# Kernel tuning notes

Measured on AMD Instinct MI355X. Metric: run time of the kernel, lower is better.

The kernel has to match this reference:

```python
import jax, jax.numpy as jnp
import numpy as np

EPSILON = 0.05
MAX_ITER = 50


def setup_inputs() -> dict:
    key = jax.random.key(0)
    k1, k2, k3 = jax.random.split(key, 3)
    B, N, M = 16, 2048, 2048
    cost = jax.random.uniform(k1, (B, N, M), dtype=jnp.float32)  # non-negative cost
    source_marginal = jax.random.uniform(k2, (B, N), dtype=jnp.float32)
    target_marginal = jax.random.uniform(k3, (B, M), dtype=jnp.float32)
    return {"cost": cost, "source_marginal": source_marginal, "target_marginal": target_marginal}


def reference(cost, source_marginal, target_marginal):
    # Log-domain Sinkhorn: fixed MAX_ITER iterations of dual updates.
    log_r = jnp.log(source_marginal + 1e-12)  # [B, N]
    log_c = jnp.log(target_marginal + 1e-12)  # [B, M]
    log_K = -cost / EPSILON                    # [B, N, M]

    log_u0 = jnp.zeros_like(log_r)
    log_v0 = jnp.zeros_like(log_c)

    def body(carry, _):
        log_u, log_v = carry
        log_u = log_r - jax.nn.logsumexp(log_K + log_v[:, None, :], axis=-1)
        log_v = log_c - jax.nn.logsumexp(log_K + log_u[:, :, None], axis=-2)
        return (log_u, log_v), None

    (log_u, log_v), _ = jax.lax.scan(body, (log_u0, log_v0), None, length=MAX_ITER)
    # Transport plan T = exp(log_u + log_K + log_v)
    return jnp.exp(log_u[:, :, None] + log_K + log_v[:, None, :])
```

## Files before the change

### kernel.cpp

```cpp
#include <hip/hip_runtime.h>
#include <cstdint>
#include <cstddef>

constexpr int B = 16, N = 2048, M = 2048;
constexpr int MAX_ITER = 50;
#define C2 (-28.853900817779268f)

constexpr int CHUNKS = 64;
constexpr int ROWS_PER_CHUNK = N / CHUNKS;

__device__ __forceinline__ unsigned short f2bf(float f) {
  union { float f; unsigned u; } x; x.f = f;
  unsigned r = x.u + 0x7fffu + ((x.u >> 16) & 1u);
  return (unsigned short)(r >> 16);
}
__device__ __forceinline__ float bflo(unsigned w) { union { unsigned u; float f; } x; x.u = w << 16; return x.f; }
__device__ __forceinline__ float bfhi(unsigned w) { union { unsigned u; float f; } x; x.u = w & 0xffff0000u; return x.f; }

__global__ __launch_bounds__(256) void init_K(const float* __restrict__ cost,
                                              uint4* __restrict__ K) {
  unsigned gid = blockIdx.x * 256u + threadIdx.x;
  const float4* c4 = (const float4*)cost;
  uint4 w0, w1;
  {
    float4 a = c4[(size_t)gid * 4 + 0];
    float4 b = c4[(size_t)gid * 4 + 1];
    w0.x = (unsigned)f2bf(exp2f(a.x * C2)) | ((unsigned)f2bf(exp2f(a.y * C2)) << 16);
    w0.y = (unsigned)f2bf(exp2f(a.z * C2)) | ((unsigned)f2bf(exp2f(a.w * C2)) << 16);
    w0.z = (unsigned)f2bf(exp2f(b.x * C2)) | ((unsigned)f2bf(exp2f(b.y * C2)) << 16);
    w0.w = (unsigned)f2bf(exp2f(b.z * C2)) | ((unsigned)f2bf(exp2f(b.w * C2)) << 16);
  }
  {
    float4 a = c4[(size_t)gid * 4 + 2];
    float4 b = c4[(size_t)gid * 4 + 3];
    w1.x = (unsigned)f2bf(exp2f(a.x * C2)) | ((unsigned)f2bf(exp2f(a.y * C2)) << 16);
    w1.y = (unsigned)f2bf(exp2f(a.z * C2)) | ((unsigned)f2bf(exp2f(a.w * C2)) << 16);
    w1.z = (unsigned)f2bf(exp2f(b.x * C2)) | ((unsigned)f2bf(exp2f(b.y * C2)) << 16);
    w1.w = (unsigned)f2bf(exp2f(b.z * C2)) | ((unsigned)f2bf(exp2f(b.w * C2)) << 16);
  }
  K[(size_t)gid * 2]     = w0;
  K[(size_t)gid * 2 + 1] = w1;
}

template <bool FIRST>
__global__ __launch_bounds__(256) void iter_fused(const uint4* __restrict__ K,
                                                  const float* __restrict__ r,
                                                  const float* __restrict__ v,
                                                  float* __restrict__ u_out,
                                                  float* __restrict__ part) {
  const int b = blockIdx.y, chunk = blockIdx.x;
  const int n0 = chunk * ROWS_PER_CHUNK;
  const int t = threadIdx.x;
  __shared__ float vs[M];
  __shared__ float us[ROWS_PER_CHUNK];

  if (FIRST) {
    float4 one; one.x = one.y = one.z = one.w = 1.0f;
    ((float4*)vs)[t] = one;
    ((float4*)vs)[t + 256] = one;
  } else {
    const float4* vv = (const float4*)(v + (size_t)b * M);
    ((float4*)vs)[t]       = vv[t];
    ((float4*)vs)[t + 256] = vv[t + 256];
  }
  __syncthreads();

  const int wave = t >> 6, lane = t & 63;
  float vreg[32];
#pragma unroll
  for (int it = 0; it < 4; ++it) {
    float4 a = ((const float4*)vs)[it * 128 + lane * 2];
    float4 c = ((const float4*)vs)[it * 128 + lane * 2 + 1];
    vreg[it * 8 + 0] = a.x; vreg[it * 8 + 1] = a.y; vreg[it * 8 + 2] = a.z; vreg[it * 8 + 3] = a.w;
    vreg[it * 8 + 4] = c.x; vreg[it * 8 + 5] = c.y; vreg[it * 8 + 6] = c.z; vreg[it * 8 + 7] = c.w;
  }

#pragma unroll
  for (int rr = 0; rr < ROWS_PER_CHUNK / 4; ++rr) {
    const int lrow = wave * (ROWS_PER_CHUNK / 4) + rr;
    const int row = n0 + lrow;
    const uint4* Kr = K + (size_t)(b * N + row) * (M / 8);
    float acc = 0.f;
#pragma unroll
    for (int it = 0; it < 4; ++it) {
      uint4 w = Kr[it * 64 + lane];
      acc += bflo(w.x) * vreg[it * 8 + 0] + bfhi(w.x) * vreg[it * 8 + 1]
           + bflo(w.y) * vreg[it * 8 + 2] + bfhi(w.y) * vreg[it * 8 + 3]
           + bflo(w.z) * vreg[it * 8 + 4] + bfhi(w.z) * vreg[it * 8 + 5]
           + bflo(w.w) * vreg[it * 8 + 6] + bfhi(w.w) * vreg[it * 8 + 7];
    }
#pragma unroll
    for (int off = 32; off; off >>= 1) acc += __shfl_xor(acc, off, 64);
    if (lane == 0) {
      float uval = (r[b * N + row] + 1e-12f) / acc;
      us[lrow] = uval;
      u_out[b * N + row] = uval;
    }
  }
  __syncthreads();

  float acc8[8] = {0, 0, 0, 0, 0, 0, 0, 0};
  const uint4* Kb = K + (size_t)(b * N + n0) * (M / 8) + t;
#pragma unroll 8
  for (int n = 0; n < ROWS_PER_CHUNK; ++n) {
    uint4 w = Kb[(size_t)n * (M / 8)];
    float uval = us[n];
    acc8[0] += bflo(w.x) * uval; acc8[1] += bfhi(w.x) * uval;
    acc8[2] += bflo(w.y) * uval; acc8[3] += bfhi(w.y) * uval;
    acc8[4] += bflo(w.z) * uval; acc8[5] += bfhi(w.z) * uval;
    acc8[6] += bflo(w.w) * uval; acc8[7] += bfhi(w.w) * uval;
  }
  float4* P = (float4*)(part + (size_t)(b * CHUNKS + chunk) * M) + t * 2;
  float4 o0; o0.x = acc8[0]; o0.y = acc8[1]; o0.z = acc8[2]; o0.w = acc8[3];
  float4 o1; o1.x = acc8[4]; o1.y = acc8[5]; o1.z = acc8[6]; o1.w = acc8[7];
  P[0] = o0; P[1] = o1;
}

__global__ __launch_bounds__(256) void v_fin(const float* __restrict__ part,
                                             const float* __restrict__ c,
                                             float* __restrict__ v) {
  const int g = blockIdx.x * 256 + threadIdx.x;
  const int b = g >> 11, m = g & (M - 1);
  float s = 0.f;
#pragma unroll 8
  for (int ch = 0; ch < CHUNKS; ++ch) s += part[(size_t)(b * CHUNKS + ch) * M + m];
  v[g] = (c[g] + 1e-12f) / s;
}

__global__ __launch_bounds__(256) void final_T(const float* __restrict__ cost,
                                               const float* __restrict__ u,
                                               const float* __restrict__ v,
                                               float* __restrict__ out) {
  const int b = blockIdx.z, n = blockIdx.y;
  const int m4 = blockIdx.x * 256 + threadIdx.x;
  const float un = u[b * N + n];
  float4 vv = ((const float4*)(v + (size_t)b * M))[m4];
  const size_t off = ((size_t)(b * N + n) * M) / 4 + m4;
  float4 cc = ((const float4*)cost)[off];
  float4 o;
  o.x = un * vv.x * exp2f(cc.x * C2);
  o.y = un * vv.y * exp2f(cc.y * C2);
  o.z = un * vv.z * exp2f(cc.z * C2);
  o.w = un * vv.w * exp2f(cc.w * C2);
  ((float4*)out)[off] = o;
}

__global__ __launch_bounds__(256) void init_v_only(float* __restrict__ v) {
  unsigned g = blockIdx.x * 256u + threadIdx.x;
  if (g < (unsigned)(B * M)) v[g] = 1.0f;
}

template <bool FIRST>
__global__ __launch_bounds__(256) void iter_fused_cost(const float* __restrict__ cost,
                                                       const float* __restrict__ r,
                                                       const float* __restrict__ v,
                                                       float* __restrict__ u_out,
                                                       float* __restrict__ part) {
  const int b = blockIdx.y, chunk = blockIdx.x;
  const int n0 = chunk * ROWS_PER_CHUNK;
  const int t = threadIdx.x;
  __shared__ float vs[M];
  __shared__ float us[ROWS_PER_CHUNK];
  if (FIRST) {
    float4 one; one.x = one.y = one.z = one.w = 1.0f;
    ((float4*)vs)[t] = one; ((float4*)vs)[t + 256] = one;
  } else {
    const float4* vv = (const float4*)(v + (size_t)b * M);
    ((float4*)vs)[t] = vv[t]; ((float4*)vs)[t + 256] = vv[t + 256];
  }
  __syncthreads();
  const int wave = t >> 6, lane = t & 63;
  float vreg[32];
#pragma unroll
  for (int it = 0; it < 4; ++it) {
    float4 a = ((const float4*)vs)[it * 128 + lane * 2];
    float4 c = ((const float4*)vs)[it * 128 + lane * 2 + 1];
    vreg[it * 8 + 0] = a.x; vreg[it * 8 + 1] = a.y; vreg[it * 8 + 2] = a.z; vreg[it * 8 + 3] = a.w;
    vreg[it * 8 + 4] = c.x; vreg[it * 8 + 5] = c.y; vreg[it * 8 + 6] = c.z; vreg[it * 8 + 7] = c.w;
  }
#pragma unroll
  for (int rr = 0; rr < ROWS_PER_CHUNK / 4; ++rr) {
    const int lrow = wave * (ROWS_PER_CHUNK / 4) + rr;
    const int row = n0 + lrow;
    const float4* Cr = (const float4*)(cost + (size_t)(b * N + row) * M);
    float acc = 0.f;
#pragma unroll
    for (int it = 0; it < 4; ++it) {
      float4 a = Cr[it * 128 + lane * 2];
      float4 c = Cr[it * 128 + lane * 2 + 1];
      acc += exp2f(a.x * C2) * vreg[it * 8 + 0] + exp2f(a.y * C2) * vreg[it * 8 + 1]
           + exp2f(a.z * C2) * vreg[it * 8 + 2] + exp2f(a.w * C2) * vreg[it * 8 + 3]
           + exp2f(c.x * C2) * vreg[it * 8 + 4] + exp2f(c.y * C2) * vreg[it * 8 + 5]
           + exp2f(c.z * C2) * vreg[it * 8 + 6] + exp2f(c.w * C2) * vreg[it * 8 + 7];
    }
#pragma unroll
    for (int off = 32; off; off >>= 1) acc += __shfl_xor(acc, off, 64);
    if (lane == 0) {
      float uval = (r[b * N + row] + 1e-12f) / acc;
      us[lrow] = uval;
      u_out[b * N + row] = uval;
    }
  }
  __syncthreads();
  float acc8[8] = {0, 0, 0, 0, 0, 0, 0, 0};
  const float4* Cb = (const float4*)(cost + (size_t)(b * N + n0) * M) + t * 2;
#pragma unroll 2
  for (int n = 0; n < ROWS_PER_CHUNK; ++n) {
    float4 a = Cb[(size_t)n * (M / 4)];
    float4 c = Cb[(size_t)n * (M / 4) + 1];
    float uval = us[n];
    acc8[0] += exp2f(a.x * C2) * uval; acc8[1] += exp2f(a.y * C2) * uval;
    acc8[2] += exp2f(a.z * C2) * uval; acc8[3] += exp2f(a.w * C2) * uval;
    acc8[4] += exp2f(c.x * C2) * uval; acc8[5] += exp2f(c.y * C2) * uval;
    acc8[6] += exp2f(c.z * C2) * uval; acc8[7] += exp2f(c.w * C2) * uval;
  }
  float4* P = (float4*)(part + (size_t)(b * CHUNKS + chunk) * M) + t * 2;
  float4 o0; o0.x = acc8[0]; o0.y = acc8[1]; o0.z = acc8[2]; o0.w = acc8[3];
  float4 o1; o1.x = acc8[4]; o1.y = acc8[5]; o1.z = acc8[6]; o1.w = acc8[7];
  P[0] = o0; P[1] = o1;
}

extern "C" void kernel_launch(void* const* d_in, const int* in_sizes, int n_in,
                              void* d_out, int out_size, void* d_ws, size_t ws_size,
                              hipStream_t stream) {
  const float* cost = (const float*)d_in[0];
  const float* r    = (const float*)d_in[1];
  const float* c    = (const float*)d_in[2];
  float* out        = (float*)d_out;
  char* ws          = (char*)d_ws;

  const size_t K_bytes    = (size_t)B * N * M * 2;
  const size_t u_bytes    = (size_t)B * N * 4;
  const size_t v_bytes    = (size_t)B * M * 4;
  const size_t part_bytes = (size_t)B * CHUNKS * M * 4;
  const size_t need_main  = K_bytes + u_bytes + v_bytes + part_bytes;
  const bool useK = (ws_size >= need_main);

  uint4* K; float *u, *v, *part;
  if (useK) {
    K = (uint4*)ws;
    u = (float*)(ws + K_bytes);
  } else {
    K = nullptr;
    u = (float*)ws;
  }
  v = u + (size_t)B * N;
  part = v + (size_t)B * M;

  if (useK) {
    init_K<<<dim3((B * (size_t)N * M) / (256 * 16)), 256, 0, stream>>>(cost, K);
    iter_fused<true><<<dim3(CHUNKS, B), 256, 0, stream>>>(K, r, v, u, part);
    v_fin<<<dim3(B * M / 256), 256, 0, stream>>>(part, c, v);
    for (int it = 1; it < MAX_ITER; ++it) {
      iter_fused<false><<<dim3(CHUNKS, B), 256, 0, stream>>>(K, r, v, u, part);
      v_fin<<<dim3(B * M / 256), 256, 0, stream>>>(part, c, v);
    }
  } else {
    iter_fused_cost<true><<<dim3(CHUNKS, B), 256, 0, stream>>>(cost, r, v, u, part);
    v_fin<<<dim3(B * M / 256), 256, 0, stream>>>(part, c, v);
    for (int it = 1; it < MAX_ITER; ++it) {
      iter_fused_cost<false><<<dim3(CHUNKS, B), 256, 0, stream>>>(cost, r, v, u, part);
      v_fin<<<dim3(B * M / 256), 256, 0, stream>>>(part, c, v);
    }
  }

  final_T<<<dim3(M / 1024, N, B), 256, 0, stream>>>(cost, u, v, out);
}
```

Baseline: 2.717 ms.

## Keep K rows in registers across row and column passes with LDS reduction

Shrinks chunks to 16 rows so each wave loads its 4 rows of bf16 K once into registers and reuses them for both the row-sum and column-sum passes. The K loads are issued before the barrier so they overlap v staging. Per-wave column partials are combined through shared memory before writing. v_fin is templated on the chunk count and uses multiple accumulators. The cost is a larger partial buffer and more v_fin reads, plus higher register pressure.

```diff
diff --git a/kernel.cpp b/kernel.cpp
--- a/kernel.cpp
+++ b/kernel.cpp
@@ -6,8 +6,8 @@
 constexpr int MAX_ITER = 50;
 #define C2 (-28.853900817779268f)
 
-constexpr int CHUNKS = 64;
-constexpr int ROWS_PER_CHUNK = N / CHUNKS;
+constexpr int ROWS_PER_CHUNK = 16;
+constexpr int CHUNKS = N / ROWS_PER_CHUNK;
 
 __device__ __forceinline__ unsigned short f2bf(float f) {
   union { float f; unsigned u; } x; x.f = f;
@@ -43,16 +43,17 @@
 }
 
 template <bool FIRST>
-__global__ __launch_bounds__(256) void iter_fused(const uint4* __restrict__ K,
-                                                  const float* __restrict__ r,
-                                                  const float* __restrict__ v,
-                                                  float* __restrict__ u_out,
-                                                  float* __restrict__ part) {
+__global__ __launch_bounds__(256, 4) void iter_fused(const uint4* __restrict__ K,
+                                                     const float* __restrict__ r,
+                                                     const float* __restrict__ v,
+                                                     float* __restrict__ u_out,
+                                                     float* __restrict__ part) {
   const int b = blockIdx.y, chunk = blockIdx.x;
   const int n0 = chunk * ROWS_PER_CHUNK;
   const int t = threadIdx.x;
-  __shared__ float vs[M];
+  __shared__ float smem[4 * 2048];
   __shared__ float us[ROWS_PER_CHUNK];
+  float* vs = smem;
 
   if (FIRST) {
     float4 one; one.x = one.y = one.z = one.w = 1.0f;
@@ -63,9 +64,19 @@
     ((float4*)vs)[t]       = vv[t];
     ((float4*)vs)[t + 256] = vv[t + 256];
   }
-  __syncthreads();
 
   const int wave = t >> 6, lane = t & 63;
+
+  uint4 kr[4][4];
+#pragma unroll
+  for (int rr = 0; rr < 4; ++rr) {
+    const uint4* Kr = K + (size_t)(b * N + n0 + wave * 4 + rr) * (M / 8);
+#pragma unroll
+    for (int it = 0; it < 4; ++it) kr[rr][it] = Kr[it * 64 + lane];
+  }
+
+  __syncthreads();
+
   float vreg[32];
 #pragma unroll
   for (int it = 0; it < 4; ++it) {
@@ -76,14 +87,11 @@
   }
 
 #pragma unroll
-  for (int rr = 0; rr < ROWS_PER_CHUNK / 4; ++rr) {
-    const int lrow = wave * (ROWS_PER_CHUNK / 4) + rr;
-    const int row = n0 + lrow;
-    const uint4* Kr = K + (size_t)(b * N + row) * (M / 8);
+  for (int rr = 0; rr < 4; ++rr) {
     float acc = 0.f;
 #pragma unroll
     for (int it = 0; it < 4; ++it) {
-      uint4 w = Kr[it * 64 + lane];
+      uint4 w = kr[rr][it];
       acc += bflo(w.x) * vreg[it * 8 + 0] + bfhi(w.x) * vreg[it * 8 + 1]
            + bflo(w.y) * vreg[it * 8 + 2] + bfhi(w.y) * vreg[it * 8 + 3]
            + bflo(w.z) * vreg[it * 8 + 4] + bfhi(w.z) * vreg[it * 8 + 5]
@@ -92,39 +100,69 @@
 #pragma unroll
     for (int off = 32; off; off >>= 1) acc += __shfl_xor(acc, off, 64);
     if (lane == 0) {
+      const int row = n0 + wave * 4 + rr;
       float uval = (r[b * N + row] + 1e-12f) / acc;
-      us[lrow] = uval;
+      us[wave * 4 + rr] = uval;
       u_out[b * N + row] = uval;
     }
   }
   __syncthreads();
 
-  float acc8[8] = {0, 0, 0, 0, 0, 0, 0, 0};
-  const uint4* Kb = K + (size_t)(b * N + n0) * (M / 8) + t;
-#pragma unroll 8
-  for (int n = 0; n < ROWS_PER_CHUNK; ++n) {
-    uint4 w = Kb[(size_t)n * (M / 8)];
-    float uval = us[n];
-    acc8[0] += bflo(w.x) * uval; acc8[1] += bfhi(w.x) * uval;
-    acc8[2] += bflo(w.y) * uval; acc8[3] += bfhi(w.y) * uval;
-    acc8[4] += bflo(w.z) * uval; acc8[5] += bfhi(w.z) * uval;
-    acc8[6] += bflo(w.w) * uval; acc8[7] += bfhi(w.w) * uval;
-  }
-  float4* P = (float4*)(part + (size_t)(b * CHUNKS + chunk) * M) + t * 2;
-  float4 o0; o0.x = acc8[0]; o0.y = acc8[1]; o0.z = acc8[2]; o0.w = acc8[3];
-  float4 o1; o1.x = acc8[4]; o1.y = acc8[5]; o1.z = acc8[6]; o1.w = acc8[7];
-  P[0] = o0; P[1] = o1;
-}
-
+  float ul[4];
+#pragma unroll
+  for (int rr = 0; rr < 4; ++rr) ul[rr] = us[wave * 4 + rr];
+
+#pragma unroll
+  for (int it = 0; it < 4; ++it) {
+    float c0 = 0, c1 = 0, c2 = 0, c3 = 0, c4 = 0, c5 = 0, c6 = 0, c7 = 0;
+#pragma unroll
+    for (int rr = 0; rr < 4; ++rr) {
+      uint4 w = kr[rr][it];
+      float uv = ul[rr];
+      c0 += bflo(w.x) * uv; c1 += bfhi(w.x) * uv;
+      c2 += bflo(w.y) * uv; c3 += bfhi(w.y) * uv;
+      c4 += bflo(w.z) * uv; c5 += bfhi(w.z) * uv;
+      c6 += bflo(w.w) * uv; c7 += bfhi(w.w) * uv;
+    }
+    float* dst = &smem[wave * 2048 + it * 512 + lane * 8];
+    float4 o0; o0.x = c0; o0.y = c1; o0.z = c2; o0.w = c3;
+    float4 o1; o1.x = c4; o1.y = c5; o1.z = c6; o1.w = c7;
+    ((float4*)dst)[0] = o0;
+    ((float4*)dst)[1] = o1;
+  }
+  __syncthreads();
+
+  const float4* cp4 = (const float4*)smem;
+  float4* Pout = (float4*)(part + (size_t)(b * CHUNKS + chunk) * M);
+#pragma unroll
+  for (int h = 0; h < 2; ++h) {
+    const int idx = h * 256 + t;
+    float4 a = cp4[idx], bb = cp4[512 + idx], cc = cp4[1024 + idx], dd = cp4[1536 + idx];
+    float4 s;
+    s.x = (a.x + bb.x) + (cc.x + dd.x);
+    s.y = (a.y + bb.y) + (cc.y + dd.y);
+    s.z = (a.z + bb.z) + (cc.z + dd.z);
+    s.w = (a.w + bb.w) + (cc.w + dd.w);
+    Pout[idx] = s;
+  }
+}
+
+template <int NCH>
 __global__ __launch_bounds__(256) void v_fin(const float* __restrict__ part,
                                              const float* __restrict__ c,
                                              float* __restrict__ v) {
   const int g = blockIdx.x * 256 + threadIdx.x;
   const int b = g >> 11, m = g & (M - 1);
-  float s = 0.f;
-#pragma unroll 8
-  for (int ch = 0; ch < CHUNKS; ++ch) s += part[(size_t)(b * CHUNKS + ch) * M + m];
-  v[g] = (c[g] + 1e-12f) / s;
+  const float* p = part + (size_t)b * NCH * M + m;
+  float s0 = 0.f, s1 = 0.f, s2 = 0.f, s3 = 0.f;
+#pragma unroll 4
+  for (int ch = 0; ch < NCH; ch += 4) {
+    s0 += p[(size_t)(ch + 0) * M];
+    s1 += p[(size_t)(ch + 1) * M];
+    s2 += p[(size_t)(ch + 2) * M];
+    s3 += p[(size_t)(ch + 3) * M];
+  }
+  v[g] = (c[g] + 1e-12f) / ((s0 + s1) + (s2 + s3));
 }
 
 __global__ __launch_bounds__(256) void final_T(const float* __restrict__ cost,
@@ -145,11 +183,6 @@
   ((float4*)out)[off] = o;
 }
 
-__global__ __launch_bounds__(256) void init_v_only(float* __restrict__ v) {
-  unsigned g = blockIdx.x * 256u + threadIdx.x;
-  if (g < (unsigned)(B * M)) v[g] = 1.0f;
-}
-
 template <bool FIRST>
 __global__ __launch_bounds__(256) void iter_fused_cost(const float* __restrict__ cost,
                                                        const float* __restrict__ r,
@@ -157,10 +190,10 @@
                                                        float* __restrict__ u_out,
                                                        float* __restrict__ part) {
   const int b = blockIdx.y, chunk = blockIdx.x;
-  const int n0 = chunk * ROWS_PER_CHUNK;
+  const int n0 = chunk * 32;
   const int t = threadIdx.x;
   __shared__ float vs[M];
-  __shared__ float us[ROWS_PER_CHUNK];
+  __shared__ float us[32];
   if (FIRST) {
     float4 one; one.x = one.y = one.z = one.w = 1.0f;
     ((float4*)vs)[t] = one; ((float4*)vs)[t + 256] = one;
@@ -179,8 +212,8 @@
     vreg[it * 8 + 4] = c.x; vreg[it * 8 + 5] = c.y; vreg[it * 8 + 6] = c.z; vreg[it * 8 + 7] = c.w;
   }
 #pragma unroll
-  for (int rr = 0; rr < ROWS_PER_CHUNK / 4; ++rr) {
-    const int lrow = wave * (ROWS_PER_CHUNK / 4) + rr;
+  for (int rr = 0; rr < 8; ++rr) {
+    const int lrow = wave * 8 + rr;
     const int row = n0 + lrow;
     const float4* Cr = (const float4*)(cost + (size_t)(b * N + row) * M);
     float acc = 0.f;
@@ -205,7 +238,7 @@
   float acc8[8] = {0, 0, 0, 0, 0, 0, 0, 0};
   const float4* Cb = (const float4*)(cost + (size_t)(b * N + n0) * M) + t * 2;
 #pragma unroll 2
-  for (int n = 0; n < ROWS_PER_CHUNK; ++n) {
+  for (int n = 0; n < 32; ++n) {
     float4 a = Cb[(size_t)n * (M / 4)];
     float4 c = Cb[(size_t)n * (M / 4) + 1];
     float uval = us[n];
@@ -214,7 +247,7 @@
     acc8[4] += exp2f(c.x * C2) * uval; acc8[5] += exp2f(c.y * C2) * uval;
     acc8[6] += exp2f(c.z * C2) * uval; acc8[7] += exp2f(c.w * C2) * uval;
   }
-  float4* P = (float4*)(part + (size_t)(b * CHUNKS + chunk) * M) + t * 2;
+  float4* P = (float4*)(part + (size_t)(b * 64 + chunk) * M) + t * 2;
   float4 o0; o0.x = acc8[0]; o0.y = acc8[1]; o0.z = acc8[2]; o0.w = acc8[3];
   float4 o1; o1.x = acc8[4]; o1.y = acc8[5]; o1.z = acc8[6]; o1.w = acc8[7];
   P[0] = o0; P[1] = o1;
@@ -250,17 +283,17 @@
   if (useK) {
     init_K<<<dim3((B * (size_t)N * M) / (256 * 16)), 256, 0, stream>>>(cost, K);
     iter_fused<true><<<dim3(CHUNKS, B), 256, 0, stream>>>(K, r, v, u, part);
-    v_fin<<<dim3(B * M / 256), 256, 0, stream>>>(part, c, v);
+    v_fin<CHUNKS><<<dim3(B * M / 256), 256, 0, stream>>>(part, c, v);
     for (int it = 1; it < MAX_ITER; ++it) {
       iter_fused<false><<<dim3(CHUNKS, B), 256, 0, stream>>>(K, r, v, u, part);
-      v_fin<<<dim3(B * M / 256), 256, 0, stream>>>(part, c, v);
+      v_fin<CHUNKS><<<dim3(B * M / 256), 256, 0, stream>>>(part, c, v);
     }
   } else {
-    iter_fused_cost<true><<<dim3(CHUNKS, B), 256, 0, stream>>>(cost, r, v, u, part);
-    v_fin<<<dim3(B * M / 256), 256, 0, stream>>>(part, c, v);
+    iter_fused_cost<true><<<dim3(64, B), 256, 0, stream>>>(cost, r, v, u, part);
+    v_fin<64><<<dim3(B * M / 256), 256, 0, stream>>>(part, c, v);
     for (int it = 1; it < MAX_ITER; ++it) {
-      iter_fused_cost<false><<<dim3(CHUNKS, B), 256, 0, stream>>>(cost, r, v, u, part);
-      v_fin<<<dim3(B * M / 256), 256, 0, stream>>>(part, c, v);
+      iter_fused_cost<false><<<dim3(64, B), 256, 0, stream>>>(cost, r, v, u, part);
+      v_fin<64><<<dim3(B * M / 256), 256, 0, stream>>>(part, c, v);
     }
   }
 
```

Result: no change. 2.698 ms (-0.7%).
